# Optimization experiments

Hardware: AMD Instinct MI355X
Metric: run time of the kernel (lower is better)

The kernel has to match this reference:

```python
import jax, jax.numpy as jnp
import numpy as np

B, F, D, K = 16384, 200, 32, 4
H1, H2 = 32, 16
BN_EPS = 1e-3  # keras BatchNormalization default epsilon


def setup_inputs() -> dict:
    key = jax.random.key(0)
    ks = jax.random.split(key, 12)
    inp = {
        "x": jax.random.normal(ks[0], (B, F, D), dtype=jnp.float32),
        "tag_embedding": jax.random.normal(ks[1], (B, D), dtype=jnp.float32),
        "vk_embs": jax.random.normal(ks[2], (D, K), dtype=jnp.float32) * 0.1,
        # tower 1: Dense(D->H1) stacked over K experts, + BN params
        "W1": jax.random.normal(ks[3], (K, D, H1), dtype=jnp.float32) * (1.0 / np.sqrt(D)),
        "b1": jnp.zeros((K, H1), dtype=jnp.float32),
        "g1": jnp.ones((K, H1), dtype=jnp.float32) + 0.1 * jax.random.normal(ks[4], (K, H1), dtype=jnp.float32),
        "be1": 0.1 * jax.random.normal(ks[5], (K, H1), dtype=jnp.float32),
        "m1": 0.1 * jax.random.normal(ks[6], (K, H1), dtype=jnp.float32),
        "v1": jax.random.uniform(ks[7], (K, H1), dtype=jnp.float32, minval=0.5, maxval=1.5),
        # tower 2: Dense(H1->H2) + BN params
        "W2": jax.random.normal(ks[8], (K, H1, H2), dtype=jnp.float32) * (1.0 / np.sqrt(H1)),
        "b2": jnp.zeros((K, H2), dtype=jnp.float32),
        "g2": jnp.ones((K, H2), dtype=jnp.float32) + 0.1 * jax.random.normal(ks[9], (K, H2), dtype=jnp.float32),
        "be2": 0.1 * jax.random.normal(ks[10], (K, H2), dtype=jnp.float32),
        "m2": 0.1 * jax.random.normal(ks[11], (K, H2), dtype=jnp.float32),
        "v2": jnp.ones((K, H2), dtype=jnp.float32),
    }
    return inp


def _bn(h, gamma, beta, mean, var):
    # inference-mode batch norm per expert, broadcast over batch: h [B,K,H]
    return (h - mean) * jax.lax.rsqrt(var + BN_EPS) * gamma + beta


def reference(x, tag_embedding, vk_embs, W1, b1, g1, be1, m1, v1,
              W2, b2, g2, be2, m2, v2):
    scale = 1.0 / jnp.sqrt(jnp.float32(D))
    # attention-pooled per-kernel context (dropout = identity in eval mode)
    vk_scores = jnp.einsum('bfd,dk->bkf', x, vk_embs)          # [B,K,F]
    vk_probs = jax.nn.softmax(vk_scores, axis=-1)
    context = jnp.einsum('bkf,bfd->bkd', vk_probs, x) * scale   # [B,K,D]
    # per-expert MLP towers, batched over K: Dense -> BN -> relu (dropout=id)
    h = jnp.einsum('bkd,kdh->bkh', context, W1) + b1            # [B,K,H1]
    h = jax.nn.relu(_bn(h, g1, be1, m1, v1))
    h = jnp.einsum('bkh,khj->bkj', h, W2) + b2                  # [B,K,H2]
    vk_outs = jax.nn.relu(_bn(h, g2, be2, m2, v2))
    # soft gate from tag embedding
    gate_scores = (tag_embedding @ vk_embs) * scale             # [B,K]
    gate_probs = jax.nn.softmax(gate_scores, axis=-1)[:, :, None]
    user_embedding = jnp.sum(vk_outs * gate_probs, axis=1)      # [B,H2]
    return user_embedding
```

## Files before the change

### kernel.cpp

```cpp
#include <hip/hip_runtime.h>
#include <hip/hip_bf16.h>

#define NF 200
#define ND 32
#define NK 4
#define NH1 32
#define NH2 16
#define BN_EPS 1e-3f

template<int CTRL>
__device__ __forceinline__ float dpp_add(float v) {
  const int r = __builtin_amdgcn_update_dpp(0, __float_as_int(v), CTRL, 0xF, 0xF, true);
  return v + __int_as_float(r);
}

__global__ __launch_bounds__(256, 8) void mvke_fused(
    const float* __restrict__ x, const float* __restrict__ tag,
    const float* __restrict__ vk,
    const float* __restrict__ W1, const float* __restrict__ b1,
    const float* __restrict__ g1, const float* __restrict__ be1,
    const float* __restrict__ m1, const float* __restrict__ v1,
    const float* __restrict__ W2, const float* __restrict__ b2,
    const float* __restrict__ g2, const float* __restrict__ be2,
    const float* __restrict__ m2, const float* __restrict__ v2,
    float* __restrict__ out, int nrows)
{
  __shared__ float w1s[NK*ND*NH1];
  __shared__ float w2s[NK*NH1*NH2];
  __shared__ float a1s[NK*NH1], c1s[NK*NH1];
  __shared__ float a2s[NK*NH2], c2s[NK*NH2];
  __shared__ float ctx_s[4][NK*ND];
  __shared__ float h1_s[4][NK*NH1];

  const int tid = threadIdx.x;
  for (int i = tid; i < NK*ND*NH1; i += 256) w1s[i] = W1[i];
  for (int i = tid; i < NK*NH1*NH2; i += 256) w2s[i] = W2[i];
  if (tid < NK*NH1) {
    const float a = g1[tid] * rsqrtf(v1[tid] + BN_EPS);
    a1s[tid] = a;
    c1s[tid] = (b1[tid] - m1[tid]) * a + be1[tid];
  } else if (tid >= 128 && tid < 128 + NK*NH2) {
    const int t = tid - 128;
    const float a = g2[t] * rsqrtf(v2[t] + BN_EPS);
    a2s[t] = a;
    c2s[t] = (b2[t] - m2[t]) * a + be2[t];
  }

  const int wave = tid >> 6;
  const int lane = tid & 63;
  const int fg   = lane >> 3;
  const int dl   = lane & 7;
  const int row  = blockIdx.x * 4 + wave;
  const bool live = (row < nrows);

  float vkt[NK][4];
  #pragma unroll
  for (int j = 0; j < 4; ++j) {
    const float4 vv = *(const float4*)(vk + (4*dl + j) * NK);
    vkt[0][j] = vv.x; vkt[1][j] = vv.y; vkt[2][j] = vv.z; vkt[3][j] = vv.w;
  }

  const float* xrow = x + (size_t)(live ? row : 0) * (NF*ND);
  const int laneoff = fg*ND + dl*4;

  float cx[NK], cy[NK], cz[NK], cw[NK], ls[NK];
  #pragma unroll
  for (int k = 0; k < NK; ++k) { cx[k]=cy[k]=cz[k]=cw[k]=ls[k]=0.f; }

  for (int it = 0; it < NF/8; ++it) {
    const float4 xa = *(const float4*)(xrow + it*(8*ND) + laneoff);
    #pragma unroll
    for (int k = 0; k < NK; ++k) {
      float t = xa.x*vkt[k][0] + xa.y*vkt[k][1] + xa.z*vkt[k][2] + xa.w*vkt[k][3];
      t = dpp_add<0xB1>(t);
      t = dpp_add<0x4E>(t);
      t = dpp_add<0x141>(t);
      const float p = __expf(t);
      ls[k] += p;
      cx[k] = fmaf(p, xa.x, cx[k]);
      cy[k] = fmaf(p, xa.y, cy[k]);
      cz[k] = fmaf(p, xa.z, cz[k]);
      cw[k] = fmaf(p, xa.w, cw[k]);
    }
  }

  #pragma unroll
  for (int k = 0; k < NK; ++k) {
    ls[k] = dpp_add<0x128>(ls[k]);
    cx[k] = dpp_add<0x128>(cx[k]);
    cy[k] = dpp_add<0x128>(cy[k]);
    cz[k] = dpp_add<0x128>(cz[k]);
    cw[k] = dpp_add<0x128>(cw[k]);
    #pragma unroll
    for (int m = 16; m <= 32; m <<= 1) {
      ls[k] += __shfl_xor(ls[k], m);
      cx[k] += __shfl_xor(cx[k], m);
      cy[k] += __shfl_xor(cy[k], m);
      cz[k] += __shfl_xor(cz[k], m);
      cw[k] += __shfl_xor(cw[k], m);
    }
  }

  const float scale = 0.17677669529663687f;
  if (fg == 0) {
    #pragma unroll
    for (int k = 0; k < NK; ++k) {
      const float inv = scale / ls[k];
      float* p = &ctx_s[wave][k*ND + dl*4];
      p[0] = cx[k]*inv; p[1] = cy[k]*inv; p[2] = cz[k]*inv; p[3] = cw[k]*inv;
    }
  }
  __syncthreads();

  #pragma unroll
  for (int rep = 0; rep < 2; ++rep) {
    const int o = lane + rep*64;
    const int k = o >> 5, h = o & 31;
    const float* wp = &w1s[k*(ND*NH1) + h];
    const float* cp = &ctx_s[wave][k*ND];
    float acc = 0.f;
    #pragma unroll
    for (int d = 0; d < ND; ++d) acc = fmaf(cp[d], wp[d*NH1], acc);
    h1_s[wave][o] = fmaxf(fmaf(acc, a1s[o], c1s[o]), 0.f);
  }
  __syncthreads();

  {
    const int k3 = lane >> 4, j3 = lane & 15;
    const float* wp = &w2s[k3*(NH1*NH2) + j3];
    const float* hp = &h1_s[wave][k3*NH1];
    float acc = 0.f;
    #pragma unroll
    for (int h = 0; h < NH1; ++h) acc = fmaf(hp[h], wp[h*NH2], acc);
    const int o = k3*NH2 + j3;
    const float h2v = fmaxf(fmaf(acc, a2s[o], c2s[o]), 0.f);

    const float* tp = tag + (size_t)(live ? row : 0) * ND;
    float gs0=0.f, gs1=0.f, gs2=0.f, gs3=0.f;
    #pragma unroll
    for (int d = 0; d < ND; ++d) {
      const float t = tp[d];
      const float4 vv = *(const float4*)(vk + d*NK);
      gs0 = fmaf(t, vv.x, gs0);
      gs1 = fmaf(t, vv.y, gs1);
      gs2 = fmaf(t, vv.z, gs2);
      gs3 = fmaf(t, vv.w, gs3);
    }
    gs0 *= scale; gs1 *= scale; gs2 *= scale; gs3 *= scale;
    const float mx = fmaxf(fmaxf(gs0, gs1), fmaxf(gs2, gs3));
    const float e0 = __expf(gs0-mx), e1 = __expf(gs1-mx),
                e2 = __expf(gs2-mx), e3 = __expf(gs3-mx);
    const float esum = e0 + e1 + e2 + e3;
    const float ek = (k3 == 0) ? e0 : (k3 == 1) ? e1 : (k3 == 2) ? e2 : e3;

    float val = (ek / esum) * h2v;
    val += __shfl_xor(val, 16);
    val += __shfl_xor(val, 32);
    if (live && lane < NH2) out[(size_t)row*NH2 + lane] = val;
  }
}

extern "C" void kernel_launch(void* const* d_in, const int* in_sizes, int n_in,
                              void* d_out, int out_size, void* d_ws, size_t ws_size,
                              hipStream_t stream) {
  const float* x   = (const float*)d_in[0];
  const float* tag = (const float*)d_in[1];
  const float* vk  = (const float*)d_in[2];
  const float* W1  = (const float*)d_in[3];
  const float* b1  = (const float*)d_in[4];
  const float* g1  = (const float*)d_in[5];
  const float* be1 = (const float*)d_in[6];
  const float* m1  = (const float*)d_in[7];
  const float* v1  = (const float*)d_in[8];
  const float* W2  = (const float*)d_in[9];
  const float* b2  = (const float*)d_in[10];
  const float* g2  = (const float*)d_in[11];
  const float* be2 = (const float*)d_in[12];
  const float* m2  = (const float*)d_in[13];
  const float* v2  = (const float*)d_in[14];
  float* out = (float*)d_out;

  const int nrows = in_sizes[1] / ND;
  const int nblocks = (nrows + 3) / 4;
  mvke_fused<<<nblocks, 256, 0, stream>>>(x, tag, vk, W1, b1, g1, be1, m1, v1,
                                          W2, b2, g2, be2, m2, v2, out, nrows);
}
```

Before: 111.5 us.

## Drop shared-memory weight staging and software-prefetch x rows

Removes the per-block copy of W1, W2 and the folded BN parameters into LDS and instead reads weights and BN params directly from global memory (L1/L2 cached) in the tower stages, computing the BN scale and shift per thread. It also double-buffers the x float4 load so the next iteration's load is issued before the current iteration's math. This cuts LDS usage and the startup copy per block, which should raise occupancy and shorten block prologue, at the cost of scattered uncached-in-LDS global reads for the small matrices.

Measured after the change: 108.0 us. -3.1%, faster.

```diff
diff --git a/kernel.cpp b/kernel.cpp
--- a/kernel.cpp
+++ b/kernel.cpp
@@ -25,27 +25,10 @@
     const float* __restrict__ m2, const float* __restrict__ v2,
     float* __restrict__ out, int nrows)
 {
-  __shared__ float w1s[NK*ND*NH1];
-  __shared__ float w2s[NK*NH1*NH2];
-  __shared__ float a1s[NK*NH1], c1s[NK*NH1];
-  __shared__ float a2s[NK*NH2], c2s[NK*NH2];
   __shared__ float ctx_s[4][NK*ND];
   __shared__ float h1_s[4][NK*NH1];
 
-  const int tid = threadIdx.x;
-  for (int i = tid; i < NK*ND*NH1; i += 256) w1s[i] = W1[i];
-  for (int i = tid; i < NK*NH1*NH2; i += 256) w2s[i] = W2[i];
-  if (tid < NK*NH1) {
-    const float a = g1[tid] * rsqrtf(v1[tid] + BN_EPS);
-    a1s[tid] = a;
-    c1s[tid] = (b1[tid] - m1[tid]) * a + be1[tid];
-  } else if (tid >= 128 && tid < 128 + NK*NH2) {
-    const int t = tid - 128;
-    const float a = g2[t] * rsqrtf(v2[t] + BN_EPS);
-    a2s[t] = a;
-    c2s[t] = (b2[t] - m2[t]) * a + be2[t];
-  }
-
+  const int tid  = threadIdx.x;
   const int wave = tid >> 6;
   const int lane = tid & 63;
   const int fg   = lane >> 3;
@@ -67,8 +50,11 @@
   #pragma unroll
   for (int k = 0; k < NK; ++k) { cx[k]=cy[k]=cz[k]=cw[k]=ls[k]=0.f; }
 
+  float4 xa = *(const float4*)(xrow + laneoff);
   for (int it = 0; it < NF/8; ++it) {
-    const float4 xa = *(const float4*)(xrow + it*(8*ND) + laneoff);
+    float4 xn;
+    if (it + 1 < NF/8)
+      xn = *(const float4*)(xrow + (it+1)*(8*ND) + laneoff);
     #pragma unroll
     for (int k = 0; k < NK; ++k) {
       float t = xa.x*vkt[k][0] + xa.y*vkt[k][1] + xa.z*vkt[k][2] + xa.w*vkt[k][3];
@@ -82,6 +68,7 @@
       cz[k] = fmaf(p, xa.z, cz[k]);
       cw[k] = fmaf(p, xa.w, cw[k]);
     }
+    xa = xn;
   }
 
   #pragma unroll
@@ -116,24 +103,28 @@
   for (int rep = 0; rep < 2; ++rep) {
     const int o = lane + rep*64;
     const int k = o >> 5, h = o & 31;
-    const float* wp = &w1s[k*(ND*NH1) + h];
+    const float* wp = W1 + k*(ND*NH1) + h;
     const float* cp = &ctx_s[wave][k*ND];
     float acc = 0.f;
     #pragma unroll
     for (int d = 0; d < ND; ++d) acc = fmaf(cp[d], wp[d*NH1], acc);
-    h1_s[wave][o] = fmaxf(fmaf(acc, a1s[o], c1s[o]), 0.f);
+    const float a = g1[o] * rsqrtf(v1[o] + BN_EPS);
+    const float c = fmaf(b1[o] - m1[o], a, be1[o]);
+    h1_s[wave][o] = fmaxf(fmaf(acc, a, c), 0.f);
   }
   __syncthreads();
 
   {
     const int k3 = lane >> 4, j3 = lane & 15;
-    const float* wp = &w2s[k3*(NH1*NH2) + j3];
+    const float* wp = W2 + k3*(NH1*NH2) + j3;
     const float* hp = &h1_s[wave][k3*NH1];
     float acc = 0.f;
     #pragma unroll
     for (int h = 0; h < NH1; ++h) acc = fmaf(hp[h], wp[h*NH2], acc);
     const int o = k3*NH2 + j3;
-    const float h2v = fmaxf(fmaf(acc, a2s[o], c2s[o]), 0.f);
+    const float a2 = g2[o] * rsqrtf(v2[o] + BN_EPS);
+    const float c2 = fmaf(b2[o] - m2[o], a2, be2[o]);
+    const float h2v = fmaxf(fmaf(acc, a2, c2), 0.f);
 
     const float* tp = tag + (size_t)(live ? row : 0) * ND;
     float gs0=0.f, gs1=0.f, gs2=0.f, gs3=0.f;
```
